# Optimization experiments

Hardware: AMD Instinct MI355X
Metric: run time of the kernel (lower is better)

## Reference

```python
import jax, jax.numpy as jnp
import numpy as np

MODEL_DIM = 2048
NUM_HEADS = 16
NUM_KV_HEADS = 4
HEAD_DIM = MODEL_DIM // NUM_HEADS  # 128
ROPE_BASE = 10000.0
LOCAL_WINDOW = 1024
EPS = 1.1920929e-07  # torch.finfo(float32).eps, F.rms_norm default
NEG = -1e30


def setup_inputs() -> dict:
    key = jax.random.key(0)
    ks = jax.random.split(key, 5)
    s = 0.02
    return {
        "x": jax.random.normal(ks[0], (1, 4096, MODEL_DIM), jnp.float32),
        "Wq": jax.random.normal(ks[1], (MODEL_DIM, MODEL_DIM), jnp.float32) * s,
        "Wk": jax.random.normal(ks[2], (NUM_KV_HEADS * HEAD_DIM, MODEL_DIM), jnp.float32) * s,
        "Wv": jax.random.normal(ks[3], (NUM_KV_HEADS * HEAD_DIM, MODEL_DIM), jnp.float32) * s,
        "Wo": jax.random.normal(ks[4], (MODEL_DIM, MODEL_DIM), jnp.float32) * s,
    }


def _rms_norm(x):
    return x * jax.lax.rsqrt(jnp.mean(x * x, axis=-1, keepdims=True) + EPS)


def _rope_tables(seqlen, dtype):
    inv_freq = 1.0 / (ROPE_BASE ** (jnp.arange(0, HEAD_DIM, 2, dtype=jnp.float32) / HEAD_DIM))
    freqs = jnp.arange(seqlen, dtype=jnp.float32)[:, None] * inv_freq[None, :]  # [S, hd/2]
    return jnp.cos(freqs).astype(dtype), jnp.sin(freqs).astype(dtype)


def _apply_rope(x, cos, sin):
    # x: [B, H, S, hd]; cos/sin: [S, hd/2]
    half = x.shape[-1] // 2
    x1, x2 = x[..., :half], x[..., half:]
    c = cos[None, None, :, :]
    s = sin[None, None, :, :]
    return jnp.concatenate((x1 * c + x2 * s, x2 * c - x1 * s), axis=-1)


def reference(x, Wq, Wk, Wv, Wo):
    B, S, _ = x.shape
    G = NUM_HEADS // NUM_KV_HEADS
    q = (x @ Wq.T).reshape(B, S, NUM_HEADS, HEAD_DIM).transpose(0, 2, 1, 3)
    k = (x @ Wk.T).reshape(B, S, NUM_KV_HEADS, HEAD_DIM).transpose(0, 2, 1, 3)
    v = (x @ Wv.T).reshape(B, S, NUM_KV_HEADS, HEAD_DIM).transpose(0, 2, 1, 3)
    q = _rms_norm(q)
    k = _rms_norm(k)
    cos, sin = _rope_tables(S, q.dtype)
    q = _apply_rope(q, cos, sin)
    k = _apply_rope(k, cos, sin)
    # GQA: expand kv heads to match query heads
    k = jnp.repeat(k, G, axis=1)  # [B, H, S, hd]
    v = jnp.repeat(v, G, axis=1)
    scale = 1.0 / np.sqrt(HEAD_DIM)
    scores = jnp.einsum("bhqd,bhkd->bhqk", q, k) * scale  # [B, H, S, S]
    idx = jnp.arange(S)
    causal = idx[None, :] <= idx[:, None]
    in_window = idx[None, :] > idx[:, None] - LOCAL_WINDOW
    allowed = causal & in_window  # [S, S]
    scores = jnp.where(allowed[None, None, :, :], scores, NEG)
    probs = jax.nn.softmax(scores, axis=-1)
    y = jnp.einsum("bhqk,bhkd->bhqd", probs, v)  # [B, H, S, hd]
    y = y.transpose(0, 2, 1, 3).reshape(B, S, MODEL_DIM)
    return y @ Wo.T
```

## Files before the change

### kernel.cpp

```cpp
#include <hip/hip_runtime.h>

typedef short bf16x8 __attribute__((ext_vector_type(8)));
typedef float f32x4 __attribute__((ext_vector_type(4)));

__device__ __forceinline__ ushort f2b(float f) {
  union { float f; unsigned u; } v; v.f = f;
  unsigned r = v.u + 0x7FFF + ((v.u >> 16) & 1);
  return (ushort)(r >> 16);
}
__device__ __forceinline__ float b2f(ushort u) {
  union { unsigned u; float f; } v; v.u = ((unsigned)u) << 16;
  return v.f;
}
__device__ __forceinline__ unsigned cvtpk(float lo, float hi) {
  unsigned r;
  asm volatile("v_cvt_pk_bf16_f32 %0, %1, %2" : "=v"(r) : "v"(lo), "v"(hi));
  return r;
}
__device__ __forceinline__ f32x4 mfma16(bf16x8 a, bf16x8 b, f32x4 c) {
  return __builtin_amdgcn_mfma_f32_16x16x32_bf16(a, b, c, 0, 0, 0);
}

#define GLD_LDS16(g, l) \
  __builtin_amdgcn_global_load_lds((const __attribute__((address_space(1))) void*)(g), \
                                   (__attribute__((address_space(3))) void*)(l), 16, 0, 0)

__global__ __launch_bounds__(256) void cast_bf16(const float* __restrict__ in,
                                                 ushort* __restrict__ out, int n4) {
  int i = blockIdx.x * 256 + threadIdx.x;
  if (i >= n4) return;
  float4 f = ((const float4*)in)[i];
  ushort4 u;
  u.x = f2b(f.x); u.y = f2b(f.y); u.z = f2b(f.z); u.w = f2b(f.w);
  ((ushort4*)out)[i] = u;
}

__global__ void rope_tables_k(float* __restrict__ cosT, float* __restrict__ sinT) {
  int s = blockIdx.x, i = threadIdx.x;
  float inv = powf(10000.0f, -(float)i * (1.0f / 64.0f));
  float f = (float)s * inv;
  cosT[s * 64 + i] = cosf(f);
  sinT[s * 64 + i] = sinf(f);
}

template <int BM, int BN, bool BF16OUT>
__global__ __launch_bounds__(512, 2) void gemm8p(const ushort* __restrict__ A,
                                                 const ushort* __restrict__ B,
                                                 void* __restrict__ Cout,
                                                 int M, int N, int K) {
  constexpr int AF = BM / 64;
  constexpr int BF = BN / 64;
  constexpr int MFR = BM / 32;
  constexpr int LA = BM / 128;
  constexpr int LB = BN / 128;
  constexpr int ASZ = BM * 32;
  constexpr int BSZ = BN * 32;
  __shared__ __align__(16) ushort lds[4 * (ASZ + BSZ)];
  const int t = threadIdx.x;
  const int lane = t & 63, w = t >> 6;
  const int wr = w & 1, wc = w >> 1;
  const int l15 = lane & 15, l4 = lane >> 4;
  const int nbn = N / BN;
  const int nwg = (int)gridDim.x;
  int bid = (int)blockIdx.x;
  bid = (bid & 7) * (nwg >> 3) + (bid >> 3);
  const long m0 = (long)(bid / nbn) * BM;
  const long n0 = (long)(bid % nbn) * BN;
  const int nk = K >> 6;
  const int rdl = (l4 * 16 + l15) * 8;

  f32x4 acc[MFR][BF] = {};
  bf16x8 af[AF], bf[BF];

#define STA(tile, ks)                                                          \
  do {                                                                         \
    const int tt_ = (tile) < nk ? (tile) : nk - 1;                             \
    _Pragma("unroll") for (int c = 0; c < LA; ++c) {                           \
      const int us_ = t * 8 + c * 4096;                                        \
      const int row_ = (us_ >> 9) * 16 + ((us_ >> 3) & 15);                    \
      const int col_ = ((us_ >> 7) & 3) * 8;                                   \
      GLD_LDS16(A + (m0 + row_) * K + tt_ * 64 + (ks) * 32 + col_,             \
                &lds[(((tile) & 1) * 2 + (ks)) * ASZ + us_]);                  \
    }                                                                          \
  } while (0)
#define STB(tile, ks)                                                          \
  do {                                                                         \
    const int tt_ = (tile) < nk ? (tile) : nk - 1;                             \
    _Pragma("unroll") for (int c = 0; c < LB; ++c) {                           \
      const int us_ = t * 8 + c * 4096;                                        \
      const int row_ = (us_ >> 9) * 16 + ((us_ >> 3) & 15);                    \
      const int col_ = ((us_ >> 7) & 3) * 8;                                   \
      GLD_LDS16(B + (n0 + row_) * K + tt_ * 64 + (ks) * 32 + col_,             \
                &lds[4 * ASZ + (((tile) & 1) * 2 + (ks)) * BSZ + us_]);        \
    }                                                                          \
  } while (0)
#define LDA8(slot, ks, mq)                                                     \
  _Pragma("unroll") for (int a = 0; a < AF; ++a)                               \
      af[a] = *(const bf16x8*)(&lds[((slot) * 2 + (ks)) * ASZ +                \
                                    (wr * MFR + (mq) * AF + a) * 512 + rdl]);
#define LDB8(slot, ks)                                                         \
  _Pragma("unroll") for (int b = 0; b < BF; ++b)                               \
      bf[b] = *(const bf16x8*)(&lds[4 * ASZ + ((slot) * 2 + (ks)) * BSZ +      \
                                    (wc * BF + b) * 512 + rdl]);
#define VMW()                                                                  \
  do {                                                                         \
    if constexpr (LA + 2 * LB == 6)                                            \
      asm volatile("s_waitcnt vmcnt(6)" ::: "memory");                         \
    else                                                                       \
      asm volatile("s_waitcnt vmcnt(5)" ::: "memory");                         \
  } while (0)
#define BARMM(mq)                                                              \
  do {                                                                         \
    __builtin_amdgcn_s_barrier();                                              \
    asm volatile("s_waitcnt lgkmcnt(0)" ::: "memory");                         \
    __builtin_amdgcn_sched_barrier(0);                                         \
    __builtin_amdgcn_s_setprio(1);                                             \
    _Pragma("unroll") for (int a = 0; a < AF; ++a)                             \
        _Pragma("unroll") for (int b = 0; b < BF; ++b)                         \
            acc[(mq) * AF + a][b] = mfma16(af[a], bf[b], acc[(mq) * AF + a][b]); \
    __builtin_amdgcn_s_setprio(0);                                             \
    __builtin_amdgcn_s_barrier();                                              \
  } while (0)

  STA(0, 0); STB(0, 0); STA(0, 1); STB(0, 1);
  STA(1, 0); STB(1, 0); STB(1, 1);
  VMW();
  __builtin_amdgcn_s_barrier();

  for (int i = 0; i < (nk >> 1); ++i) {
    const int t1 = 2 * i + 1, t2 = 2 * i + 2, t3 = 2 * i + 3;
    LDA8(0, 0, 0); LDB8(0, 0); STA(t1, 1);          BARMM(0);
    LDA8(0, 0, 1);             STB(t2, 0);          BARMM(1);
    LDA8(0, 1, 0); LDB8(0, 1); STA(t2, 0);          BARMM(0);
    LDA8(0, 1, 1);             STB(t2, 1); VMW();   BARMM(1);
    LDA8(1, 0, 0); LDB8(1, 0); STA(t2, 1);          BARMM(0);
    LDA8(1, 0, 1);             STB(t3, 0);          BARMM(1);
    LDA8(1, 1, 0); LDB8(1, 1); STA(t3, 0);          BARMM(0);
    LDA8(1, 1, 1);             STB(t3, 1); VMW();   BARMM(1);
  }
  asm volatile("s_waitcnt vmcnt(0)" ::: "memory");

#pragma unroll
  for (int m = 0; m < MFR; ++m) {
#pragma unroll
    for (int n = 0; n < BF; ++n) {
      long mrow = m0 + wr * (BM / 2) + m * 16 + l4 * 4;
      long ncol = n0 + wc * (BN / 4) + n * 16 + l15;
#pragma unroll
      for (int r = 0; r < 4; ++r) {
        if constexpr (BF16OUT)
          ((ushort*)Cout)[(mrow + r) * N + ncol] = f2b(acc[m][n][r]);
        else
          ((float*)Cout)[(mrow + r) * N + ncol] = acc[m][n][r];
      }
    }
  }
#undef STA
#undef STB
#undef LDA8
#undef LDB8
#undef VMW
#undef BARMM
}

__global__ __launch_bounds__(256) void postproc_k(const ushort* __restrict__ qkvb,
                                                  const float* __restrict__ cosT,
                                                  const float* __restrict__ sinT,
                                                  ushort* __restrict__ qb,
                                                  ushort* __restrict__ kb,
                                                  ushort* __restrict__ vtb) {
  const int lane = threadIdx.x & 63;
  const int s = blockIdx.x * 4 + (threadIdx.x >> 6);
  const int h = blockIdx.y;
  const int colbase = (h < 16) ? h * 128 : (h < 20 ? 2048 + (h - 16) * 128
                                                   : 2560 + (h - 20) * 128);
  const ushort* row = qkvb + (long)s * 3072 + colbase;
  float x1 = b2f(row[lane]), x2 = b2f(row[lane + 64]);
  if (h >= 20) {
    int kvh = h - 20;
    int spos = (s & ~31) | (((s >> 2) & 3) * 8 + ((s >> 4) & 1) * 4 + (s & 3));
    vtb[(long)(kvh * 128 + lane) * 4096 + spos]      = f2b(x1);
    vtb[(long)(kvh * 128 + lane + 64) * 4096 + spos] = f2b(x2);
    return;
  }
  float ss = x1 * x1 + x2 * x2;
#pragma unroll
  for (int m = 1; m < 64; m <<= 1) ss += __shfl_xor(ss, m);
  float rn = rsqrtf(ss * (1.0f / 128.0f) + 1.1920929e-07f);
  float c = cosT[s * 64 + lane], sn = sinT[s * 64 + lane];
  float x1n = x1 * rn, x2n = x2 * rn;
  float o1 = x1n * c + x2n * sn;
  float o2 = x2n * c - x1n * sn;
  if (h < 16) {
    const float scq = 0.08838834764831845f;
    ushort* dst = qb + ((long)h * 4096 + s) * 128;
    dst[lane] = f2b(o1 * scq);
    dst[lane + 64] = f2b(o2 * scq);
  } else {
    ushort* dst = kb + ((long)(h - 16) * 4096 + s) * 128;
    dst[lane] = f2b(o1);
    dst[lane + 64] = f2b(o2);
  }
}

__global__ __launch_bounds__(512) void attn_k(const ushort* __restrict__ qb,
                                              const ushort* __restrict__ kb,
                                              const ushort* __restrict__ vtb,
                                              ushort* __restrict__ yb) {
  __shared__ __align__(16) ushort lds[32768];
  const int t = threadIdx.x;
  const int lane = t & 63, w = t >> 6;
  const int l15 = lane & 15, l4 = lane >> 4;
  const int q0 = ((int)gridDim.x - 1 - (int)blockIdx.x) * 128;
  const int h = blockIdx.y, kvh = h >> 2;
  const int qw = q0 + w * 16;
  const int q = qw + l15;

  const ushort* Qp = qb + ((long)h * 4096 + q) * 128 + l4 * 8;
  bf16x8 qf[4];
#pragma unroll
  for (int c = 0; c < 4; ++c) qf[c] = *(const bf16x8*)(Qp + c * 32);

  const ushort* Kg = kb + (long)kvh * 4096 * 128;
  const ushort* Vg = vtb + (long)kvh * 128 * 4096;

  int kb_lo = q0 - 1023; if (kb_lo < 0) kb_lo = 0; kb_lo &= ~63;
  const int nt = (q0 + 127 - kb_lo) / 64 + 1;

  const int lbuA = w * 512 + lane * 8;
  const int lbuB = lbuA + 4096;
  const int krA = ((lbuA >> 9) >> 2) * 16 + ((lbuA >> 3) & 15);
  const int kcA = ((lbuA >> 9) & 3) * 32 + ((lbuA >> 7) & 3) * 8;
  const int krB = ((lbuB >> 9) >> 2) * 16 + ((lbuB >> 3) & 15);
  const int kcB = ((lbuB >> 9) & 3) * 32 + ((lbuB >> 7) & 3) * 8;
  const int vrA = ((lbuA >> 9) >> 1) * 16 + ((lbuA >> 5) & 15);
  const int vcA = ((lbuA >> 9) & 1) * 32 + ((lbuA >> 3) & 3) * 8;
  const int vrB = ((lbuB >> 9) >> 1) * 16 + ((lbuB >> 5) & 15);
  const int vcB = ((lbuB >> 9) & 1) * 32 + ((lbuB >> 3) & 3) * 8;

#define STAGE(kbs, b)                                                        \
  do {                                                                       \
    ushort* Kl_ = &lds[(b) * 16384];                                         \
    ushort* Vl_ = &lds[(b) * 16384 + 8192];                                  \
    GLD_LDS16(Kg + (long)((kbs) + krA) * 128 + kcA, Kl_ + lbuA);             \
    GLD_LDS16(Kg + (long)((kbs) + krB) * 128 + kcB, Kl_ + lbuB);             \
    GLD_LDS16(Vg + (long)vrA * 4096 + (kbs) + vcA, Vl_ + lbuA);              \
    GLD_LDS16(Vg + (long)vrB * 4096 + (kbs) + vcB, Vl_ + lbuB);              \
  } while (0)

  f32x4 o[8] = {};
  float mrun = -1e30f, lrun = 0.0f;

  STAGE(kb_lo, 0);
  asm volatile("s_waitcnt vmcnt(0)" ::: "memory");
  __syncthreads();

  for (int ti = 0; ti < nt; ++ti) {
    const int kbs = kb_lo + ti * 64;
    const int cur = ti & 1;
    if (ti + 1 < nt) STAGE(kbs + 64, cur ^ 1);

    if (kbs + 63 >= qw - 1023 && kbs <= qw + 15) {
      const ushort* Kl = &lds[cur * 16384];
      const ushort* Vl = &lds[cur * 16384 + 8192];
      const int rdl = (l4 * 16 + l15) * 8;

      f32x4 sc[4];
#pragma unroll
      for (int st = 0; st < 4; ++st) {
        sc[st] = f32x4{0.f, 0.f, 0.f, 0.f};
#pragma unroll
        for (int c = 0; c < 4; ++c)
          sc[st] = mfma16(*(const bf16x8*)(Kl + (st * 4 + c) * 512 + rdl),
                          qf[c], sc[st]);
      }

      const bool full = (kbs + 64 <= qw) && (kbs >= qw - 1008);
      float s[16];
      if (full) {
#pragma unroll
        for (int st = 0; st < 4; ++st)
#pragma unroll
          for (int r = 0; r < 4; ++r) s[st * 4 + r] = sc[st][r];
      } else {
#pragma unroll
        for (int st = 0; st < 4; ++st)
#pragma unroll
          for (int r = 0; r < 4; ++r) {
            const int ki = kbs + st * 16 + l4 * 4 + r;
            s[st * 4 + r] = (ki <= q && ki > q - 1024) ? sc[st][r] : -1e30f;
          }
      }

      float m0a = fmaxf(fmaxf(s[0], s[1]), fmaxf(s[2], s[3]));
      float m1a = fmaxf(fmaxf(s[4], s[5]), fmaxf(s[6], s[7]));
      float m2a = fmaxf(fmaxf(s[8], s[9]), fmaxf(s[10], s[11]));
      float m3a = fmaxf(fmaxf(s[12], s[13]), fmaxf(s[14], s[15]));
      float mx = fmaxf(fmaxf(m0a, m1a), fmaxf(m2a, m3a));
      mx = fmaxf(mx, __shfl_xor(mx, 16));
      mx = fmaxf(mx, __shfl_xor(mx, 32));

      float mn;
      if (__all(mx <= mrun + 8.0f)) {
        mn = mrun;
      } else {
        mn = fmaxf(mrun, mx);
        const float corr = __expf(mrun - mn);
        mrun = mn;
#pragma unroll
        for (int db = 0; db < 8; ++db)
#pragma unroll
          for (int r = 0; r < 4; ++r) o[db][r] *= corr;
        lrun *= corr;
      }

      float p[16];
#pragma unroll
      for (int j = 0; j < 16; ++j) p[j] = __expf(s[j] - mn);
      float ps = ((p[0] + p[1]) + (p[2] + p[3])) + ((p[4] + p[5]) + (p[6] + p[7]));
      ps += ((p[8] + p[9]) + (p[10] + p[11])) + ((p[12] + p[13]) + (p[14] + p[15]));
      ps += __shfl_xor(ps, 16);
      ps += __shfl_xor(ps, 32);
      lrun += ps;

      union { unsigned u[4]; bf16x8 v; } pa, pb;
      pa.u[0] = cvtpk(p[0], p[1]);   pa.u[1] = cvtpk(p[2], p[3]);
      pa.u[2] = cvtpk(p[4], p[5]);   pa.u[3] = cvtpk(p[6], p[7]);
      pb.u[0] = cvtpk(p[8], p[9]);   pb.u[1] = cvtpk(p[10], p[11]);
      pb.u[2] = cvtpk(p[12], p[13]); pb.u[3] = cvtpk(p[14], p[15]);

      const int vbase = l15 * 32 + l4 * 8;
#pragma unroll
      for (int db = 0; db < 8; ++db) {
        const ushort* vrp = Vl + db * 1024 + vbase;
        o[db] = mfma16(*(const bf16x8*)vrp, pa.v, o[db]);
        o[db] = mfma16(*(const bf16x8*)(vrp + 512), pb.v, o[db]);
      }
    }
    __syncthreads();
  }

  const float inv = 1.0f / lrun;
#pragma unroll
  for (int db = 0; db < 8; ++db)
#pragma unroll
    for (int r = 0; r < 4; ++r)
      yb[(long)q * 2048 + h * 128 + db * 16 + l4 * 4 + r] = f2b(o[db][r] * inv);
}

extern "C" void kernel_launch(void* const* d_in, const int* in_sizes, int n_in,
                              void* d_out, int out_size, void* d_ws, size_t ws_size,
                              hipStream_t stream) {
  (void)in_sizes; (void)n_in; (void)out_size; (void)ws_size;
  const float* x  = (const float*)d_in[0];
  const float* Wq = (const float*)d_in[1];
  const float* Wk = (const float*)d_in[2];
  const float* Wv = (const float*)d_in[3];
  const float* Wo = (const float*)d_in[4];
  const long S = 4096;
  ushort* ws   = (ushort*)d_ws;
  ushort* xb   = ws;
  ushort* wqkv = xb + S * 2048;
  ushort* wob  = wqkv + 3072L * 2048;
  ushort* qkvb = wob + 2048L * 2048;
  ushort* qb   = qkvb + S * 3072;
  ushort* kbuf = qb + S * 2048;
  ushort* vtb  = kbuf + 4L * 4096 * 128;
  ushort* yb   = vtb + 4L * 128 * 4096;
  float* cosT  = (float*)(yb + S * 2048);
  float* sinT  = cosT + S * 64;

  cast_bf16<<<dim3(8192), 256, 0, stream>>>(x, xb, (int)(S * 2048 / 4));
  cast_bf16<<<dim3(4096), 256, 0, stream>>>(Wq, wqkv, 2048 * 2048 / 4);
  cast_bf16<<<dim3(1024), 256, 0, stream>>>(Wk, wqkv + 2048L * 2048, 512 * 2048 / 4);
  cast_bf16<<<dim3(1024), 256, 0, stream>>>(Wv, wqkv + 2560L * 2048, 512 * 2048 / 4);
  cast_bf16<<<dim3(4096), 256, 0, stream>>>(Wo, wob, 2048 * 2048 / 4);

  gemm8p<256, 256, true><<<dim3(192), 512, 0, stream>>>(xb, wqkv, qkvb, 4096, 3072, 2048);
  rope_tables_k<<<dim3(4096), 64, 0, stream>>>(cosT, sinT);
  postproc_k<<<dim3(1024, 24), 256, 0, stream>>>(qkvb, cosT, sinT, qb, kbuf, vtb);
  attn_k<<<dim3(32, 16), 512, 0, stream>>>(qb, kbuf, vtb, yb);
  gemm8p<128, 256, false><<<dim3(256), 512, 0, stream>>>(yb, wob, d_out, 4096, 2048, 2048);
}
```

Before: 225.1 us.

## Replace 8-phase big-tile GEMM with simpler 128x128 double-buffered GEMM and fuse casts

Result: slower. 275.5 us (+22.4%).

```diff
diff --git a/kernel.cpp b/kernel.cpp
--- a/kernel.cpp
+++ b/kernel.cpp
@@ -25,14 +25,33 @@
   __builtin_amdgcn_global_load_lds((const __attribute__((address_space(1))) void*)(g), \
                                    (__attribute__((address_space(3))) void*)(l), 16, 0, 0)
 
-__global__ __launch_bounds__(256) void cast_bf16(const float* __restrict__ in,
-                                                 ushort* __restrict__ out, int n4) {
-  int i = blockIdx.x * 256 + threadIdx.x;
-  if (i >= n4) return;
-  float4 f = ((const float4*)in)[i];
+__global__ __launch_bounds__(256) void cast_all(const float* __restrict__ x,
+                                                const float* __restrict__ wq,
+                                                const float* __restrict__ wk,
+                                                const float* __restrict__ wv,
+                                                const float* __restrict__ wo,
+                                                ushort* __restrict__ xb,
+                                                ushort* __restrict__ wqkvb,
+                                                ushort* __restrict__ wob) {
+  const long i = (long)blockIdx.x * 256 + threadIdx.x;
+  const float* src;
+  ushort* dst;
+  long j;
+  if (i < 2097152) {
+    src = x; j = i; dst = xb;
+  } else if (i < 3145728) {
+    src = wq; j = i - 2097152; dst = wqkvb;
+  } else if (i < 3407872) {
+    src = wk; j = i - 3145728; dst = wqkvb + 4194304;
+  } else if (i < 3670016) {
+    src = wv; j = i - 3407872; dst = wqkvb + 5242880;
+  } else {
+    src = wo; j = i - 3670016; dst = wob;
+  }
+  float4 f = ((const float4*)src)[j];
   ushort4 u;
   u.x = f2b(f.x); u.y = f2b(f.y); u.z = f2b(f.z); u.w = f2b(f.w);
-  ((ushort4*)out)[i] = u;
+  ((ushort4*)dst)[j] = u;
 }
 
 __global__ void rope_tables_k(float* __restrict__ cosT, float* __restrict__ sinT) {
@@ -43,124 +62,94 @@
   sinT[s * 64 + i] = sinf(f);
 }
 
-template <int BM, int BN, bool BF16OUT>
-__global__ __launch_bounds__(512, 2) void gemm8p(const ushort* __restrict__ A,
-                                                 const ushort* __restrict__ B,
-                                                 void* __restrict__ Cout,
-                                                 int M, int N, int K) {
-  constexpr int AF = BM / 64;
-  constexpr int BF = BN / 64;
-  constexpr int MFR = BM / 32;
-  constexpr int LA = BM / 128;
-  constexpr int LB = BN / 128;
-  constexpr int ASZ = BM * 32;
-  constexpr int BSZ = BN * 32;
-  __shared__ __align__(16) ushort lds[4 * (ASZ + BSZ)];
+template <bool BF16OUT>
+__global__ __launch_bounds__(256) void gemm2b(const ushort* __restrict__ A,
+                                              const ushort* __restrict__ B,
+                                              void* __restrict__ Cout,
+                                              int M, int N, int K) {
+  __shared__ __align__(16) ushort As[2][8192];
+  __shared__ __align__(16) ushort Bs[2][8192];
   const int t = threadIdx.x;
   const int lane = t & 63, w = t >> 6;
   const int wr = w & 1, wc = w >> 1;
   const int l15 = lane & 15, l4 = lane >> 4;
-  const int nbn = N / BN;
+  const int nbn = N >> 7;
   const int nwg = (int)gridDim.x;
   int bid = (int)blockIdx.x;
   bid = (bid & 7) * (nwg >> 3) + (bid >> 3);
-  const long m0 = (long)(bid / nbn) * BM;
-  const long n0 = (long)(bid % nbn) * BN;
+  const long m0 = (long)(bid / nbn) * 128;
+  const long n0 = (long)(bid % nbn) * 128;
   const int nk = K >> 6;
-  const int rdl = (l4 * 16 + l15) * 8;
-
-  f32x4 acc[MFR][BF] = {};
-  bf16x8 af[AF], bf[BF];
-
-#define STA(tile, ks)                                                          \
+
+  int srow[4], scol[4];
+#pragma unroll
+  for (int c = 0; c < 4; ++c) {
+    const int us = t * 8 + c * 2048;
+    srow[c] = ((us >> 9) >> 1) * 16 + ((us >> 3) & 15);
+    scol[c] = ((us >> 9) & 1) * 32 + ((us >> 7) & 3) * 8;
+  }
+
+#define STG(tile, slot)                                                        \
   do {                                                                         \
-    const int tt_ = (tile) < nk ? (tile) : nk - 1;                             \
-    _Pragma("unroll") for (int c = 0; c < LA; ++c) {                           \
-      const int us_ = t * 8 + c * 4096;                                        \
-      const int row_ = (us_ >> 9) * 16 + ((us_ >> 3) & 15);                    \
-      const int col_ = ((us_ >> 7) & 3) * 8;                                   \
-      GLD_LDS16(A + (m0 + row_) * K + tt_ * 64 + (ks) * 32 + col_,             \
-                &lds[(((tile) & 1) * 2 + (ks)) * ASZ + us_]);                  \
-    }                                                                          \
+    _Pragma("unroll") for (int c = 0; c < 4; ++c)                              \
+        GLD_LDS16(A + (m0 + srow[c]) * K + (tile) * 64 + scol[c],              \
+                  &As[slot][t * 8 + c * 2048]);                                \
+    _Pragma("unroll") for (int c = 0; c < 4; ++c)                              \
+        GLD_LDS16(B + (n0 + srow[c]) * K + (tile) * 64 + scol[c],              \
+                  &Bs[slot][t * 8 + c * 2048]);                                \
   } while (0)
-#define STB(tile, ks)                                                          \
-  do {                                                                         \
-    const int tt_ = (tile) < nk ? (tile) : nk - 1;                             \
-    _Pragma("unroll") for (int c = 0; c < LB; ++c) {                           \
-      const int us_ = t * 8 + c * 4096;                                        \
-      const int row_ = (us_ >> 9) * 16 + ((us_ >> 3) & 15);                    \
-      const int col_ = ((us_ >> 7) & 3) * 8;                                   \
-      GLD_LDS16(B + (n0 + row_) * K + tt_ * 64 + (ks) * 32 + col_,             \
-                &lds[4 * ASZ + (((tile) & 1) * 2 + (ks)) * BSZ + us_]);        \
-    }                                                                          \
-  } while (0)
-#define LDA8(slot, ks, mq)                                                     \
-  _Pragma("unroll") for (int a = 0; a < AF; ++a)                               \
-      af[a] = *(const bf16x8*)(&lds[((slot) * 2 + (ks)) * ASZ +                \
-                                    (wr * MFR + (mq) * AF + a) * 512 + rdl]);
-#define LDB8(slot, ks)                                                         \
-  _Pragma("unroll") for (int b = 0; b < BF; ++b)                               \
-      bf[b] = *(const bf16x8*)(&lds[4 * ASZ + ((slot) * 2 + (ks)) * BSZ +      \
-                                    (wc * BF + b) * 512 + rdl]);
-#define VMW()                                                                  \
-  do {                                                                         \
-    if constexpr (LA + 2 * LB == 6)                                            \
-      asm volatile("s_waitcnt vmcnt(6)" ::: "memory");                         \
-    else                                                                       \
-      asm volatile("s_waitcnt vmcnt(5)" ::: "memory");                         \
-  } while (0)
-#define BARMM(mq)                                                              \
-  do {                                                                         \
-    __builtin_amdgcn_s_barrier();                                              \
-    asm volatile("s_waitcnt lgkmcnt(0)" ::: "memory");                         \
-    __builtin_amdgcn_sched_barrier(0);                                         \
-    __builtin_amdgcn_s_setprio(1);                                             \
-    _Pragma("unroll") for (int a = 0; a < AF; ++a)                             \
-        _Pragma("unroll") for (int b = 0; b < BF; ++b)                         \
-            acc[(mq) * AF + a][b] = mfma16(af[a], bf[b], acc[(mq) * AF + a][b]); \
-    __builtin_amdgcn_s_setprio(0);                                             \
-    __builtin_amdgcn_s_barrier();                                              \
-  } while (0)
-
-  STA(0, 0); STB(0, 0); STA(0, 1); STB(0, 1);
-  STA(1, 0); STB(1, 0); STB(1, 1);
-  VMW();
-  __builtin_amdgcn_s_barrier();
-
-  for (int i = 0; i < (nk >> 1); ++i) {
-    const int t1 = 2 * i + 1, t2 = 2 * i + 2, t3 = 2 * i + 3;
-    LDA8(0, 0, 0); LDB8(0, 0); STA(t1, 1);          BARMM(0);
-    LDA8(0, 0, 1);             STB(t2, 0);          BARMM(1);
-    LDA8(0, 1, 0); LDB8(0, 1); STA(t2, 0);          BARMM(0);
-    LDA8(0, 1, 1);             STB(t2, 1); VMW();   BARMM(1);
-    LDA8(1, 0, 0); LDB8(1, 0); STA(t2, 1);          BARMM(0);
-    LDA8(1, 0, 1);             STB(t3, 0);          BARMM(1);
-    LDA8(1, 1, 0); LDB8(1, 1); STA(t3, 0);          BARMM(0);
-    LDA8(1, 1, 1);             STB(t3, 1); VMW();   BARMM(1);
+
+  f32x4 acc[4][4] = {};
+  STG(0, 0);
+
+  for (int j = 0; j < nk; ++j) {
+    const int kn = (j + 1 < nk) ? j + 1 : nk - 1;
+    STG(kn, (j + 1) & 1);
+    asm volatile("s_waitcnt vmcnt(8)" ::: "memory");
+    __builtin_amdgcn_s_barrier();
+    const int sl = j & 1;
+    bf16x8 af[4][2], bf[4][2];
+#pragma unroll
+    for (int mf = 0; mf < 4; ++mf)
+#pragma unroll
+      for (int ks = 0; ks < 2; ++ks)
+        af[mf][ks] = *(const bf16x8*)(&As[sl][((wr * 4 + mf) * 2 + ks) * 512 + lane * 8]);
+#pragma unroll
+    for (int nf = 0; nf < 4; ++nf)
+#pragma unroll
+      for (int ks = 0; ks < 2; ++ks)
+        bf[nf][ks] = *(const bf16x8*)(&Bs[sl][((wc * 4 + nf) * 2 + ks) * 512 + lane * 8]);
+    asm volatile("s_waitcnt lgkmcnt(0)" ::: "memory");
+    __builtin_amdgcn_sched_barrier(0);
+    __builtin_amdgcn_s_setprio(1);
+#pragma unroll
+    for (int mf = 0; mf < 4; ++mf)
+#pragma unroll
+      for (int nf = 0; nf < 4; ++nf)
+#pragma unroll
+        for (int ks = 0; ks < 2; ++ks)
+          acc[mf][nf] = mfma16(af[mf][ks], bf[nf][ks], acc[mf][nf]);
+    __builtin_amdgcn_s_setprio(0);
+    __builtin_amdgcn_s_barrier();
   }
   asm volatile("s_waitcnt vmcnt(0)" ::: "memory");
 
 #pragma unroll
-  for (int m = 0; m < MFR; ++m) {
-#pragma unroll
-    for (int n = 0; n < BF; ++n) {
-      long mrow = m0 + wr * (BM / 2) + m * 16 + l4 * 4;
-      long ncol = n0 + wc * (BN / 4) + n * 16 + l15;
+  for (int mf = 0; mf < 4; ++mf) {
+#pragma unroll
+    for (int nf = 0; nf < 4; ++nf) {
+      long mrow = m0 + wr * 64 + mf * 16 + l4 * 4;
+      long ncol = n0 + wc * 64 + nf * 16 + l15;
 #pragma unroll
       for (int r = 0; r < 4; ++r) {
         if constexpr (BF16OUT)
-          ((ushort*)Cout)[(mrow + r) * N + ncol] = f2b(acc[m][n][r]);
+          ((ushort*)Cout)[(mrow + r) * N + ncol] = f2b(acc[mf][nf][r]);
         else
-          ((float*)Cout)[(mrow + r) * N + ncol] = acc[m][n][r];
+          ((float*)Cout)[(mrow + r) * N + ncol] = acc[mf][nf][r];
       }
     }
   }
-#undef STA
-#undef STB
-#undef LDA8
-#undef LDB8
-#undef VMW
-#undef BARMM
+#undef STG
 }
 
 __global__ __launch_bounds__(256) void postproc_k(const ushort* __restrict__ qkvb,
@@ -370,15 +359,10 @@
   float* cosT  = (float*)(yb + S * 2048);
   float* sinT  = cosT + S * 64;
 
-  cast_bf16<<<dim3(8192), 256, 0, stream>>>(x, xb, (int)(S * 2048 / 4));
-  cast_bf16<<<dim3(4096), 256, 0, stream>>>(Wq, wqkv, 2048 * 2048 / 4);
-  cast_bf16<<<dim3(1024), 256, 0, stream>>>(Wk, wqkv + 2048L * 2048, 512 * 2048 / 4);
-  cast_bf16<<<dim3(1024), 256, 0, stream>>>(Wv, wqkv + 2560L * 2048, 512 * 2048 / 4);
-  cast_bf16<<<dim3(4096), 256, 0, stream>>>(Wo, wob, 2048 * 2048 / 4);
-
-  gemm8p<256, 256, true><<<dim3(192), 512, 0, stream>>>(xb, wqkv, qkvb, 4096, 3072, 2048);
+  cast_all<<<dim3(18432), 256, 0, stream>>>(x, Wq, Wk, Wv, Wo, xb, wqkv, wob);
+  gemm2b<true><<<dim3(32 * 24), 256, 0, stream>>>(xb, wqkv, qkvb, 4096, 3072, 2048);
   rope_tables_k<<<dim3(4096), 64, 0, stream>>>(cosT, sinT);
   postproc_k<<<dim3(1024, 24), 256, 0, stream>>>(qkvb, cosT, sinT, qb, kbuf, vtb);
   attn_k<<<dim3(32, 16), 512, 0, stream>>>(qb, kbuf, vtb, yb);
-  gemm8p<128, 256, false><<<dim3(256), 512, 0, stream>>>(yb, wob, d_out, 4096, 2048, 2048);
-}
+  gemm2b<false><<<dim3(32 * 16), 256, 0, stream>>>(yb, wob, d_out, 4096, 2048, 2048);
+}
```
